# Kernel optimization log

Hardware: AMD Instinct MI355X
Metric: run time of the kernel (lower is better)

Reference implementation:

```python
import jax, jax.numpy as jnp
import numpy as np

B, H, L = 32768, 768, 10

def setup_inputs() -> dict:
    key = jax.random.key(0)
    ks = jax.random.split(key, 9)
    return {
        "hidden_state": jax.random.normal(ks[0], (B, H), dtype=jnp.float32),
        "w1": jax.random.normal(ks[1], (L, H), dtype=jnp.float32) * 0.02,
        "b1": jax.random.normal(ks[2], (L,), dtype=jnp.float32) * 0.02,
        "w2": jax.random.normal(ks[3], (L, H), dtype=jnp.float32) * 0.02,
        "b2": jax.random.normal(ks[4], (L,), dtype=jnp.float32) * 0.02,
        "w3": jax.random.normal(ks[5], (L, H), dtype=jnp.float32) * 0.02,
        "b3": jax.random.normal(ks[6], (L,), dtype=jnp.float32) * 0.02,
        "groups": jax.random.randint(ks[7], (B,), 0, 3, dtype=jnp.int32),
        "labels": jax.random.randint(ks[8], (B,), 0, L, dtype=jnp.int32),
    }

def reference(hidden_state, w1, b1, w2, b2, w3, b3, groups, labels):
    # Fused: run all 3 heads as one batched GEMM -> [B, 3, L]
    W = jnp.stack([w1, w2, w3])          # [3, L, H]
    bias = jnp.stack([b1, b2, b3])       # [3, L]
    logits3 = jnp.einsum('bh,glh->bgl', hidden_state, W) + bias[None, :, :]
    # Per-sample group selection (vectorized gather, replaces Python loop)
    logits = jnp.take_along_axis(logits3, groups[:, None, None].astype(jnp.int32), axis=1)[:, 0, :]  # [B, L]
    # Cross-entropy with mean reduction (nn.CrossEntropyLoss default)
    logp = jax.nn.log_softmax(logits, axis=-1)
    nll = -jnp.take_along_axis(logp, labels[:, None].astype(jnp.int32), axis=1)[:, 0]
    return jnp.mean(nll)
```

## Files before the change

kernel.cpp:

```cpp
#include <hip/hip_runtime.h>
#include <hip/hip_bf16.h>

#define B_N 32768
#define H_N 768
#define L_N 10
#define M_BLK 32
#define NCOL 32
#define NSLOT 96
#define KQ_STEPS 6

typedef __attribute__((ext_vector_type(8))) short short8v;
typedef __attribute__((ext_vector_type(4))) float float4v;

static __device__ __forceinline__ short8v cvt8(const float4 f0, const float4 f1) {
    union { __hip_bfloat162 h[4]; short8v v; } u;
    u.h[0] = __float22bfloat162_rn(make_float2(f0.x, f0.y));
    u.h[1] = __float22bfloat162_rn(make_float2(f0.z, f0.w));
    u.h[2] = __float22bfloat162_rn(make_float2(f1.x, f1.y));
    u.h[3] = __float22bfloat162_rn(make_float2(f1.z, f1.w));
    return u.v;
}

__global__ __launch_bounds__(256) void prep_weights(
    const float* __restrict__ w1, const float* __restrict__ w2,
    const float* __restrict__ w3, short* __restrict__ wb)
{
    const int idx = blockIdx.x * 256 + threadIdx.x;
    if (idx >= NSLOT * NCOL) return;
    const int slot = idx >> 5;
    const int c    = idx & 31;
    short8v v;
    if (c < 30) {
        const float* src = (c < 10) ? (w1 + c * H_N)
                         : (c < 20) ? (w2 + (c - 10) * H_N)
                                    : (w3 + (c - 20) * H_N);
        const float4 f0 = *reinterpret_cast<const float4*>(src + slot * 8);
        const float4 f1 = *reinterpret_cast<const float4*>(src + slot * 8 + 4);
        v = cvt8(f0, f1);
    } else {
        v = short8v{0, 0, 0, 0, 0, 0, 0, 0};
    }
    *reinterpret_cast<short8v*>(wb + idx * 8) = v;
}

__global__ __launch_bounds__(512) void fused_mfma_ce(
    const float* __restrict__ hs, const short* __restrict__ wb,
    const float* __restrict__ b1v, const float* __restrict__ b2v,
    const float* __restrict__ b3v,
    const int* __restrict__ groups, const int* __restrict__ labels,
    float* __restrict__ out)
{
    __shared__ float slog[4][M_BLK][33];

    const int t  = threadIdx.x;
    const int w  = t >> 6;
    const int mt = w & 1;
    const int kq = w >> 1;
    const int l  = t & 63;
    const int cq = l & 15;
    const int bq = l >> 4;

    const int m0 = blockIdx.x * M_BLK + mt * 16;
    const float* aptr = hs + (size_t)(m0 + cq) * H_N + kq * (H_N / 4) + bq * 8;
    const short* bb0 = wb + (((kq * KQ_STEPS * 4 + bq) * NCOL) + cq) * 8;
    const short* bb1 = bb0 + 16 * 8;

    float4v acc0 = {0.f, 0.f, 0.f, 0.f};
    float4v acc1 = {0.f, 0.f, 0.f, 0.f};

    #pragma unroll 2
    for (int ks = 0; ks < KQ_STEPS; ++ks) {
        const float4 f0 = *reinterpret_cast<const float4*>(aptr + ks * 32);
        const float4 f1 = *reinterpret_cast<const float4*>(aptr + ks * 32 + 4);
        const short8v b0 = *reinterpret_cast<const short8v*>(bb0 + ks * (NCOL * 4 * 8));
        const short8v b1 = *reinterpret_cast<const short8v*>(bb1 + ks * (NCOL * 4 * 8));
        const short8v a = cvt8(f0, f1);
        acc0 = __builtin_amdgcn_mfma_f32_16x16x32_bf16(a, b0, acc0, 0, 0, 0);
        acc1 = __builtin_amdgcn_mfma_f32_16x16x32_bf16(a, b1, acc1, 0, 0, 0);
    }

    #pragma unroll
    for (int r = 0; r < 4; ++r) {
        slog[kq][mt * 16 + bq * 4 + r][cq]      = acc0[r];
        slog[kq][mt * 16 + bq * 4 + r][cq + 16] = acc1[r];
    }
    __syncthreads();

    float nll = 0.f;
    if (t < M_BLK) {
        const int s   = blockIdx.x * M_BLK + t;
        const int g   = groups[s];
        const int lab = labels[s];
        const float* bp = (g == 0) ? b1v : ((g == 1) ? b2v : b3v);
        float lv[L_N];
        #pragma unroll
        for (int j = 0; j < L_N; ++j)
            lv[j] = slog[0][t][g * 10 + j] + slog[1][t][g * 10 + j]
                  + slog[2][t][g * 10 + j] + slog[3][t][g * 10 + j] + bp[j];
        float m = lv[0];
        #pragma unroll
        for (int j = 1; j < L_N; ++j) m = fmaxf(m, lv[j]);
        float sum = 0.f;
        #pragma unroll
        for (int j = 0; j < L_N; ++j) sum += expf(lv[j] - m);
        float sel = lv[0];
        #pragma unroll
        for (int j = 1; j < L_N; ++j) sel = (lab == j) ? lv[j] : sel;
        nll = (m + logf(sum)) - sel;
    }
    if (t < 64) {
        #pragma unroll
        for (int off = 32; off > 0; off >>= 1)
            nll += __shfl_down(nll, off, 64);
        if (t == 0) atomicAdd(out, nll * (1.0f / (float)B_N));
    }
}

extern "C" void kernel_launch(void* const* d_in, const int* in_sizes, int n_in,
                              void* d_out, int out_size, void* d_ws, size_t ws_size,
                              hipStream_t stream) {
    const float* hs  = (const float*)d_in[0];
    const float* w1  = (const float*)d_in[1];
    const float* b1v = (const float*)d_in[2];
    const float* w2  = (const float*)d_in[3];
    const float* b2v = (const float*)d_in[4];
    const float* w3  = (const float*)d_in[5];
    const float* b3v = (const float*)d_in[6];
    const int* groups = (const int*)d_in[7];
    const int* labels = (const int*)d_in[8];
    float* out = (float*)d_out;
    short* wb  = (short*)d_ws;

    hipMemsetAsync(out, 0, sizeof(float), stream);
    prep_weights<<<(NSLOT * NCOL + 255) / 256, 256, 0, stream>>>(w1, w2, w3, wb);
    fused_mfma_ce<<<B_N / M_BLK, 512, 0, stream>>>(
        hs, wb, b1v, b2v, b3v, groups, labels, out);
}
```

Measured before the change: 36.04 us.

## Split K in halves, preload all A loads upfront, stage bf16 weights in LDS

```diff
diff --git a/kernel.cpp b/kernel.cpp
--- a/kernel.cpp
+++ b/kernel.cpp
@@ -7,7 +7,7 @@
 #define M_BLK 32
 #define NCOL 32
 #define NSLOT 96
-#define KQ_STEPS 6
+#define KH_STEPS 12
 
 typedef __attribute__((ext_vector_type(8))) short short8v;
 typedef __attribute__((ext_vector_type(4))) float float4v;
@@ -43,46 +43,62 @@
     *reinterpret_cast<short8v*>(wb + idx * 8) = v;
 }
 
-__global__ __launch_bounds__(512) void fused_mfma_ce(
+__global__ __launch_bounds__(256) void fused_mfma_ce(
     const float* __restrict__ hs, const short* __restrict__ wb,
     const float* __restrict__ b1v, const float* __restrict__ b2v,
     const float* __restrict__ b3v,
     const int* __restrict__ groups, const int* __restrict__ labels,
     float* __restrict__ out)
 {
-    __shared__ float slog[4][M_BLK][33];
+    __shared__ __align__(16) short wlds[NSLOT * NCOL * 8];
 
     const int t  = threadIdx.x;
     const int w  = t >> 6;
     const int mt = w & 1;
-    const int kq = w >> 1;
+    const int kh = w >> 1;
     const int l  = t & 63;
     const int cq = l & 15;
     const int bq = l >> 4;
 
     const int m0 = blockIdx.x * M_BLK + mt * 16;
-    const float* aptr = hs + (size_t)(m0 + cq) * H_N + kq * (H_N / 4) + bq * 8;
-    const short* bb0 = wb + (((kq * KQ_STEPS * 4 + bq) * NCOL) + cq) * 8;
+    const float* aptr = hs + (size_t)(m0 + cq) * H_N + kh * (H_N / 2) + bq * 8;
+
+    float4 aA[KH_STEPS], aB[KH_STEPS];
+    #pragma unroll
+    for (int i = 0; i < KH_STEPS; ++i) {
+        aA[i] = *reinterpret_cast<const float4*>(aptr + i * 32);
+        aB[i] = *reinterpret_cast<const float4*>(aptr + i * 32 + 4);
+    }
+
+    {
+        const short8v* src = reinterpret_cast<const short8v*>(wb);
+        short8v* dst = reinterpret_cast<short8v*>(wlds);
+        for (int idx = t; idx < NSLOT * NCOL; idx += 256)
+            dst[idx] = src[idx];
+    }
+    __syncthreads();
+
+    const short* bb0 = wlds + (((kh * KH_STEPS * 4 + bq) * NCOL) + cq) * 8;
     const short* bb1 = bb0 + 16 * 8;
 
     float4v acc0 = {0.f, 0.f, 0.f, 0.f};
     float4v acc1 = {0.f, 0.f, 0.f, 0.f};
 
-    #pragma unroll 2
-    for (int ks = 0; ks < KQ_STEPS; ++ks) {
-        const float4 f0 = *reinterpret_cast<const float4*>(aptr + ks * 32);
-        const float4 f1 = *reinterpret_cast<const float4*>(aptr + ks * 32 + 4);
+    #pragma unroll
+    for (int ks = 0; ks < KH_STEPS; ++ks) {
         const short8v b0 = *reinterpret_cast<const short8v*>(bb0 + ks * (NCOL * 4 * 8));
         const short8v b1 = *reinterpret_cast<const short8v*>(bb1 + ks * (NCOL * 4 * 8));
-        const short8v a = cvt8(f0, f1);
+        const short8v a = cvt8(aA[ks], aB[ks]);
         acc0 = __builtin_amdgcn_mfma_f32_16x16x32_bf16(a, b0, acc0, 0, 0, 0);
         acc1 = __builtin_amdgcn_mfma_f32_16x16x32_bf16(a, b1, acc1, 0, 0, 0);
     }
 
+    __syncthreads();
+    float (*slog)[M_BLK][33] = (float (*)[M_BLK][33])wlds;
     #pragma unroll
     for (int r = 0; r < 4; ++r) {
-        slog[kq][mt * 16 + bq * 4 + r][cq]      = acc0[r];
-        slog[kq][mt * 16 + bq * 4 + r][cq + 16] = acc1[r];
+        slog[kh][mt * 16 + bq * 4 + r][cq]      = acc0[r];
+        slog[kh][mt * 16 + bq * 4 + r][cq + 16] = acc1[r];
     }
     __syncthreads();
 
@@ -95,8 +111,7 @@
         float lv[L_N];
         #pragma unroll
         for (int j = 0; j < L_N; ++j)
-            lv[j] = slog[0][t][g * 10 + j] + slog[1][t][g * 10 + j]
-                  + slog[2][t][g * 10 + j] + slog[3][t][g * 10 + j] + bp[j];
+            lv[j] = slog[0][t][g * 10 + j] + slog[1][t][g * 10 + j] + bp[j];
         float m = lv[0];
         #pragma unroll
         for (int j = 1; j < L_N; ++j) m = fmaxf(m, lv[j]);
@@ -133,6 +148,6 @@
 
     hipMemsetAsync(out, 0, sizeof(float), stream);
     prep_weights<<<(NSLOT * NCOL + 255) / 256, 256, 0, stream>>>(w1, w2, w3, wb);
-    fused_mfma_ce<<<B_N / M_BLK, 512, 0, stream>>>(
+    fused_mfma_ce<<<B_N / M_BLK, 256, 0, stream>>>(
         hs, wb, b1v, b2v, b3v, groups, labels, out);
 }
```

New measurement: 40.93 us. +13.6%, slower.
